# Performance work log

Hardware: AMD Instinct MI355X
Metric: run time of the kernel (lower is better)

The kernel has to match this reference:

```python
import jax, jax.numpy as jnp
import numpy as np

N, E = 50000, 400000          # nodes, edges
T, R = 4, 8                   # node types, relations (edge types)
H, DK = 8, 32                 # heads, head dim
DIN = DOUT = 256              # in/out feature dim (DOUT = H*DK)
SQRT_DK = float(np.sqrt(DK))


def setup_inputs() -> dict:
    key = jax.random.key(0)
    ks = jax.random.split(key, 12)
    f32 = jnp.float32
    return {
        "x": jax.random.normal(ks[0], (N, DIN), f32),
        "node_type": jax.random.randint(ks[1], (N,), 0, T, jnp.int32),
        "src": jax.random.randint(ks[2], (E,), 0, N, jnp.int32),
        "dst": jax.random.randint(ks[3], (E,), 0, N, jnp.int32),
        "etype": jax.random.randint(ks[4], (E,), 0, R, jnp.int32),
        "Wk": jax.random.normal(ks[5], (T, DOUT, DIN), f32) / np.sqrt(DIN).astype(np.float32),
        "bk": jnp.zeros((T, DOUT), f32),
        "Wq": jax.random.normal(ks[6], (T, DOUT, DIN), f32) / np.sqrt(DIN).astype(np.float32),
        "bq": jnp.zeros((T, DOUT), f32),
        "Wv": jax.random.normal(ks[7], (T, DOUT, DIN), f32) / np.sqrt(DIN).astype(np.float32),
        "bv": jnp.zeros((T, DOUT), f32),
        "Wa": jax.random.normal(ks[8], (T, DOUT, DOUT), f32) / np.sqrt(DOUT).astype(np.float32),
        "ba": jnp.zeros((T, DOUT), f32),
        "rel_pri": jnp.ones((R, H), f32),
        "rel_att": jax.random.normal(ks[9], (R, H, DK, DK), f32) / np.sqrt(DK).astype(np.float32),  # ~xavier
        "rel_msg": jax.random.normal(ks[10], (R, H, DK, DK), f32) / np.sqrt(DK).astype(np.float32),
        "skip": jnp.ones((T,), f32),
    }


def _typed_linear(h, W, b, ntype):
    # per-node-type linear: y_n = W[type_n] @ h_n + b[type_n]
    y = jnp.einsum('ni,tdi->ntd', h, W)                      # [N,T,D] (T is small)
    y = jnp.take_along_axis(y, ntype[:, None, None], axis=1)[:, 0]
    return y + b[ntype]


def _hgt_forward(x, node_type, src, dst, etype,
                 Wk, bk, Wq, bq, Wv, bv, Wa, ba,
                 rel_pri, rel_att, rel_msg, skip):
    # typed k/q/v projections -> [N,H,DK]
    K = _typed_linear(x, Wk, bk, node_type).reshape(N, H, DK)
    Q = _typed_linear(x, Wq, bq, node_type).reshape(N, H, DK)
    V = _typed_linear(x, Wv, bv, node_type).reshape(N, H, DK)

    k_e, q_e, v_e = K[src], Q[dst], V[src]                   # [E,H,DK] gathers

    # per-relation head transforms (loop over small fixed R, masked accumulate)
    key_e = jnp.zeros_like(k_e)
    msg_e = jnp.zeros_like(v_e)
    for r in range(R):
        m = (etype == r)[:, None, None].astype(x.dtype)
        key_e = key_e + m * jnp.einsum('ehd,hdf->ehf', k_e, rel_att[r])
        msg_e = msg_e + m * jnp.einsum('ehd,hdf->ehf', v_e, rel_msg[r])

    att = (q_e * key_e).sum(-1) * rel_pri[etype] / SQRT_DK   # [E,H]

    # softmax per (dst node, edge type) segment, then mean across edge types
    seg = dst * R + etype                                    # [E]
    S = N * R
    amax = jax.ops.segment_max(att, seg, num_segments=S)     # [S,H]
    ex = jnp.exp(att - amax[seg])
    denom = jax.ops.segment_sum(ex, seg, num_segments=S)
    w = ex / denom[seg]                                      # normalized attention [E,H]
    h_seg = jax.ops.segment_sum(w[:, :, None] * msg_e, seg, num_segments=S)  # [S,H,DK]
    cnt = jax.ops.segment_sum(jnp.ones((E,), x.dtype), seg, num_segments=S)  # [S]

    h_nr = h_seg.reshape(N, R, DOUT)
    present = (cnt.reshape(N, R) > 0).astype(x.dtype)        # which etypes hit each node
    t = h_nr.sum(1) / jnp.maximum(present.sum(1), 1.0)[:, None]  # cross_reducer='mean'

    trans = _typed_linear(t, Wa, ba, node_type)              # per-type output linear
    alpha = jax.nn.sigmoid(skip)[node_type][:, None]
    return trans * alpha + x * (1.0 - alpha)


def reference(x, node_type, src, dst, etype,
              Wk, bk, Wq, bq, Wv, bv, Wa, ba,
              rel_pri, rel_att, rel_msg, skip):
    return _hgt_forward(x, node_type, src, dst, etype,
                        Wk, bk, Wq, bq, Wv, bv, Wa, ba,
                        rel_pri, rel_att, rel_msg, skip)
```

## Files before the change

kernel.cpp:

```cpp
#include <hip/hip_runtime.h>
#include <math.h>
#include <stdint.h>

#define N_NODES 50000
#define N_EDGES 400000
#define N_T 4
#define N_R 8
#define N_H 8
#define DKD 32
#define D 256
#define TM 64
#define N_SEG (N_NODES * N_R)
#define PROJ_BLOCKS ((N_NODES + TM - 1) / TM + N_T)

typedef _Float16 h2 __attribute__((ext_vector_type(2)));
typedef _Float16 v8h __attribute__((ext_vector_type(8)));
typedef float v4f __attribute__((ext_vector_type(4)));
typedef unsigned short u16;

__device__ __forceinline__ u16 h2u(_Float16 h) { return __builtin_bit_cast(u16, h); }
__device__ __forceinline__ h2 u2h2(unsigned int u) { return __builtin_bit_cast(h2, u); }

#if __has_builtin(__builtin_amdgcn_fdot2)
__device__ __forceinline__ float fdot2f(h2 a, h2 b, float c) {
    return __builtin_amdgcn_fdot2(a, b, c, false);
}
#else
__device__ __forceinline__ float fdot2f(h2 a, h2 b, float c) {
    return c + (float)a[0] * (float)b[0] + (float)a[1] * (float)b[1];
}
#endif

__device__ __forceinline__ unsigned int pk16(float a, float b) {
#if __has_builtin(__builtin_amdgcn_cvt_pkrtz)
    return __builtin_bit_cast(unsigned int, __builtin_amdgcn_cvt_pkrtz(a, b));
#else
    return __builtin_bit_cast(unsigned int, h2{(_Float16)a, (_Float16)b});
#endif
}

struct Q4 { uint4 a, b, c, d; };

__device__ __forceinline__ float dot32q(const uint4* __restrict__ m, const Q4& q) {
    uint4 m0 = m[0], m1 = m[1], m2 = m[2], m3 = m[3];
    float s = 0.f;
    s = fdot2f(u2h2(m0.x), u2h2(q.a.x), s);
    s = fdot2f(u2h2(m0.y), u2h2(q.a.y), s);
    s = fdot2f(u2h2(m0.z), u2h2(q.a.z), s);
    s = fdot2f(u2h2(m0.w), u2h2(q.a.w), s);
    s = fdot2f(u2h2(m1.x), u2h2(q.b.x), s);
    s = fdot2f(u2h2(m1.y), u2h2(q.b.y), s);
    s = fdot2f(u2h2(m1.z), u2h2(q.b.z), s);
    s = fdot2f(u2h2(m1.w), u2h2(q.b.w), s);
    s = fdot2f(u2h2(m2.x), u2h2(q.c.x), s);
    s = fdot2f(u2h2(m2.y), u2h2(q.c.y), s);
    s = fdot2f(u2h2(m2.z), u2h2(q.c.z), s);
    s = fdot2f(u2h2(m2.w), u2h2(q.c.w), s);
    s = fdot2f(u2h2(m3.x), u2h2(q.d.x), s);
    s = fdot2f(u2h2(m3.y), u2h2(q.d.y), s);
    s = fdot2f(u2h2(m3.z), u2h2(q.d.z), s);
    s = fdot2f(u2h2(m3.w), u2h2(q.d.w), s);
    return s;
}

__global__ __launch_bounds__(256) void k_cvtW(
    const float4* __restrict__ w0, const float4* __restrict__ w1,
    const float4* __restrict__ w2, const float4* __restrict__ w3,
    ushort4* __restrict__ d, int n4each) {
    int i = blockIdx.x * 256 + threadIdx.x;
    if (i >= 4 * n4each) return;
    int sel = i / n4each, j = i - sel * n4each;
    const float4* s = (sel == 0) ? w0 : (sel == 1) ? w1 : (sel == 2) ? w2 : w3;
    float4 v = s[j];
    ushort4 o;
    o.x = h2u((_Float16)v.x); o.y = h2u((_Float16)v.y);
    o.z = h2u((_Float16)v.z); o.w = h2u((_Float16)v.w);
    d[i] = o;
}

__global__ __launch_bounds__(256) void k_cvt_att(const float4* __restrict__ s,
                                                 const float* __restrict__ pri,
                                                 ushort4* __restrict__ d, int n4) {
    int i = blockIdx.x * 256 + threadIdx.x;
    if (i >= n4) return;
    int mat = i >> 8;
    float sc = pri[mat] * 0.2550309305920868f;
    float4 v = s[i];
    ushort4 o;
    o.x = h2u((_Float16)(v.x * sc)); o.y = h2u((_Float16)(v.y * sc));
    o.z = h2u((_Float16)(v.z * sc)); o.w = h2u((_Float16)(v.w * sc));
    d[i] = o;
}

__global__ __launch_bounds__(256) void k_cvt_t(const float* __restrict__ s,
                                               u16* __restrict__ d) {
    int i = blockIdx.x * 256 + threadIdx.x;
    if (i >= N_R * N_H * DKD * DKD) return;
    int mat = i >> 10, w = i & 1023;
    int d0 = w >> 5, f = w & 31;
    d[(mat << 10) + f * DKD + d0] = h2u((_Float16)s[i]);
}

__global__ void k_hist(const int* __restrict__ nt, int* __restrict__ cnt) {
    int n = blockIdx.x * blockDim.x + threadIdx.x;
    if (n < N_NODES) atomicAdd(&cnt[nt[n]], 1);
}

__global__ void k_scan(const int* __restrict__ cnt, int* __restrict__ off,
                       int* __restrict__ toff) {
    int o = 0, to = 0;
    for (int t = 0; t < N_T; t++) {
        off[t] = o; toff[t] = to;
        o += cnt[t]; to += (cnt[t] + TM - 1) / TM;
    }
    off[N_T] = o; toff[N_T] = to;
}

__global__ void k_scatter(const int* __restrict__ nt, const int* __restrict__ off,
                          int* __restrict__ cur, int* __restrict__ order) {
    int n = blockIdx.x * blockDim.x + threadIdx.x;
    if (n >= N_NODES) return;
    int t = nt[n];
    int pos = off[t] + atomicAdd(&cur[t], 1);
    order[pos] = n;
}

__global__ void k_hist_seg(const int* __restrict__ dst, const int* __restrict__ et,
                           int* __restrict__ cnt) {
    int e = blockIdx.x * blockDim.x + threadIdx.x;
    if (e < N_EDGES) atomicAdd(&cnt[dst[e] * N_R + et[e]], 1);
}

__global__ __launch_bounds__(1024) void k_scan_l1(const int* __restrict__ cnt,
                                                  int* __restrict__ excl,
                                                  int* __restrict__ bsum) {
    __shared__ int sh[1024];
    int tid = threadIdx.x, i = blockIdx.x * 1024 + tid;
    int v = (i < N_SEG) ? cnt[i] : 0;
    sh[tid] = v;
    __syncthreads();
    #pragma unroll
    for (int ofs = 1; ofs < 1024; ofs <<= 1) {
        int t = (tid >= ofs) ? sh[tid - ofs] : 0;
        __syncthreads();
        sh[tid] += t;
        __syncthreads();
    }
    if (i < N_SEG) excl[i] = sh[tid] - v;
    if (tid == 1023) bsum[blockIdx.x] = sh[1023];
}

__global__ __launch_bounds__(512) void k_scan_l2(int* __restrict__ bsum, int NB) {
    __shared__ int sh[512];
    int tid = threadIdx.x;
    int v = (tid < NB) ? bsum[tid] : 0;
    sh[tid] = v;
    __syncthreads();
    #pragma unroll
    for (int ofs = 1; ofs < 512; ofs <<= 1) {
        int t = (tid >= ofs) ? sh[tid - ofs] : 0;
        __syncthreads();
        sh[tid] += t;
        __syncthreads();
    }
    if (tid < NB) bsum[tid] = sh[tid] - v;
}

__global__ void k_scan_l3(int* __restrict__ excl, const int* __restrict__ bsum) {
    int i = blockIdx.x * blockDim.x + threadIdx.x;
    if (i < N_SEG) excl[i] += bsum[i >> 10];
    else if (i == N_SEG) excl[N_SEG] = N_EDGES;
}

__global__ void k_scatter_seg(const int* __restrict__ src, const int* __restrict__ dst,
                              const int* __restrict__ et, const int* __restrict__ rp,
                              int* __restrict__ cur, int* __restrict__ esrc) {
    int e = blockIdx.x * blockDim.x + threadIdx.x;
    if (e >= N_EDGES) return;
    int sg = dst[e] * N_R + et[e];
    int pos = rp[sg] + atomicAdd(&cur[sg], 1);
    esrc[pos] = src[e];
}

__global__ __launch_bounds__(256) void k_proj(
    const float* __restrict__ x, const int* __restrict__ order,
    const int* __restrict__ off, const int* __restrict__ toff,
    const u16* __restrict__ Wkb, const float* __restrict__ bk,
    const u16* __restrict__ Wqb, const float* __restrict__ bq,
    const u16* __restrict__ Wvb, const float* __restrict__ bv,
    u16* __restrict__ Kb, u16* __restrict__ Qb, u16* __restrict__ Vb) {
    __shared__ __align__(16) u16 xs[TM][D + 8];
    int b = blockIdx.x;
    int t = -1;
    #pragma unroll
    for (int i = 0; i < N_T; i++)
        if (b >= toff[i] && b < toff[i + 1]) t = i;
    if (t < 0) return;
    int nodeBase = off[t] + (b - toff[t]) * TM;
    int count = min(TM, off[t + 1] - nodeBase);
    int tid = threadIdx.x;

    for (int j = tid; j < TM * (D / 4); j += 256) {
        int row = j >> 6, ch = j & 63;
        float4 v = {0.f, 0.f, 0.f, 0.f};
        if (row < count) {
            int g = order[nodeBase + row];
            v = *(const float4*)(x + (size_t)g * D + ch * 4);
        }
        ushort4 o;
        o.x = h2u((_Float16)v.x); o.y = h2u((_Float16)v.y);
        o.z = h2u((_Float16)v.z); o.w = h2u((_Float16)v.w);
        *(ushort4*)&xs[row][ch * 4] = o;
    }
    __syncthreads();

    int lane = tid & 63, wave = tid >> 6;
    int m = lane & 15, quad = lane >> 4;
    v8h a[8];
    #pragma unroll
    for (int ks = 0; ks < 8; ks++)
        a[ks] = *(const v8h*)&xs[wave * 16 + m][ks * 32 + quad * 8];

    int grow[4]; bool vrow[4];
    #pragma unroll
    for (int r = 0; r < 4; r++) {
        int rowi = wave * 16 + quad * 4 + r;
        vrow[r] = (rowi < count);
        grow[r] = vrow[r] ? order[nodeBase + rowi] : 0;
    }

    const u16* Ws[3] = {Wkb + (size_t)t * D * D, Wqb + (size_t)t * D * D, Wvb + (size_t)t * D * D};
    const float* Bs[3] = {bk + t * D, bq + t * D, bv + t * D};
    u16* Os[3] = {Kb, Qb, Vb};

    for (int p = 0; p < 3; p++) {
        const u16* W = Ws[p];
        for (int dt = 0; dt < 16; dt++) {
            int dcol = dt * 16 + m;
            v4f acc = {0.f, 0.f, 0.f, 0.f};
            #pragma unroll
            for (int ks = 0; ks < 8; ks++) {
                v8h bf = *(const v8h*)(W + (size_t)dcol * D + ks * 32 + quad * 8);
                acc = __builtin_amdgcn_mfma_f32_16x16x32_f16(a[ks], bf, acc, 0, 0, 0);
            }
            float bias = Bs[p][dcol];
            #pragma unroll
            for (int r = 0; r < 4; r++) {
                if (vrow[r])
                    Os[p][(size_t)grow[r] * D + dcol] = h2u((_Float16)(acc[r] + bias));
            }
        }
    }
}

__global__ __launch_bounds__(256) void k_fused(
    const u16* __restrict__ Kb, u16* QTb, const u16* __restrict__ Vb,
    const int* __restrict__ rowptr, const int* __restrict__ esrc,
    const u16* __restrict__ Ab, const u16* __restrict__ Mtb) {
    int tid = threadIdx.x;
    int n = blockIdx.x * 32 + (tid >> 3);
    if (n >= N_NODES) return;
    int h = tid & 7;
    int base = n * N_R;
    u16* qrow = QTb + (size_t)n * D + h * DKD;

    float macc[DKD];
    #pragma unroll
    for (int j = 0; j < DKD; j++) macc[j] = 0.f;
    float np = 0.f;

    int s0 = rowptr[base];
    for (int r = 0; r < N_R; r++) {
        int s1 = rowptr[base + r + 1];
        if (s0 < s1) {
            np += 1.f;
            Q4 q4;
            {
                const uint4* qp = (const uint4*)qrow;
                q4.a = qp[0]; q4.b = qp[1]; q4.c = qp[2]; q4.d = qp[3];
            }
            const uint4* Ar = (const uint4*)(Ab + ((size_t)(r * N_H + h) << 10));
            Q4 qt;
            {
                float t0, t1;
                t0 = dot32q(Ar + 0, q4);  t1 = dot32q(Ar + 4, q4);  qt.a.x = pk16(t0, t1);
                t0 = dot32q(Ar + 8, q4);  t1 = dot32q(Ar + 12, q4); qt.a.y = pk16(t0, t1);
                t0 = dot32q(Ar + 16, q4); t1 = dot32q(Ar + 20, q4); qt.a.z = pk16(t0, t1);
                t0 = dot32q(Ar + 24, q4); t1 = dot32q(Ar + 28, q4); qt.a.w = pk16(t0, t1);
                t0 = dot32q(Ar + 32, q4); t1 = dot32q(Ar + 36, q4); qt.b.x = pk16(t0, t1);
                t0 = dot32q(Ar + 40, q4); t1 = dot32q(Ar + 44, q4); qt.b.y = pk16(t0, t1);
                t0 = dot32q(Ar + 48, q4); t1 = dot32q(Ar + 52, q4); qt.b.z = pk16(t0, t1);
                t0 = dot32q(Ar + 56, q4); t1 = dot32q(Ar + 60, q4); qt.b.w = pk16(t0, t1);
                t0 = dot32q(Ar + 64, q4); t1 = dot32q(Ar + 68, q4); qt.c.x = pk16(t0, t1);
                t0 = dot32q(Ar + 72, q4); t1 = dot32q(Ar + 76, q4); qt.c.y = pk16(t0, t1);
                t0 = dot32q(Ar + 80, q4); t1 = dot32q(Ar + 84, q4); qt.c.z = pk16(t0, t1);
                t0 = dot32q(Ar + 88, q4); t1 = dot32q(Ar + 92, q4); qt.c.w = pk16(t0, t1);
                t0 = dot32q(Ar + 96, q4); t1 = dot32q(Ar + 100, q4); qt.d.x = pk16(t0, t1);
                t0 = dot32q(Ar + 104, q4); t1 = dot32q(Ar + 108, q4); qt.d.y = pk16(t0, t1);
                t0 = dot32q(Ar + 112, q4); t1 = dot32q(Ar + 116, q4); qt.d.z = pk16(t0, t1);
                t0 = dot32q(Ar + 120, q4); t1 = dot32q(Ar + 124, q4); qt.d.w = pk16(t0, t1);
            }
            float den = 0.f;
            float U[DKD];
            #pragma unroll
            for (int j = 0; j < DKD; j++) U[j] = 0.f;
            for (int e = s0; e < s1; e++) {
                int s = esrc[e];
                const uint4* kp = (const uint4*)(Kb + (size_t)s * D + h * DKD);
                const uint4* vp = (const uint4*)(Vb + (size_t)s * D + h * DKD);
                Q4 kv; kv.a = kp[0]; kv.b = kp[1]; kv.c = kp[2]; kv.d = kp[3];
                uint4 v0 = vp[0], v1 = vp[1], v2 = vp[2], v3 = vp[3];
                float p = 0.f;
                p = fdot2f(u2h2(kv.a.x), u2h2(qt.a.x), p);
                p = fdot2f(u2h2(kv.a.y), u2h2(qt.a.y), p);
                p = fdot2f(u2h2(kv.a.z), u2h2(qt.a.z), p);
                p = fdot2f(u2h2(kv.a.w), u2h2(qt.a.w), p);
                p = fdot2f(u2h2(kv.b.x), u2h2(qt.b.x), p);
                p = fdot2f(u2h2(kv.b.y), u2h2(qt.b.y), p);
                p = fdot2f(u2h2(kv.b.z), u2h2(qt.b.z), p);
                p = fdot2f(u2h2(kv.b.w), u2h2(qt.b.w), p);
                p = fdot2f(u2h2(kv.c.x), u2h2(qt.c.x), p);
                p = fdot2f(u2h2(kv.c.y), u2h2(qt.c.y), p);
                p = fdot2f(u2h2(kv.c.z), u2h2(qt.c.z), p);
                p = fdot2f(u2h2(kv.c.w), u2h2(qt.c.w), p);
                p = fdot2f(u2h2(kv.d.x), u2h2(qt.d.x), p);
                p = fdot2f(u2h2(kv.d.y), u2h2(qt.d.y), p);
                p = fdot2f(u2h2(kv.d.z), u2h2(qt.d.z), p);
                p = fdot2f(u2h2(kv.d.w), u2h2(qt.d.w), p);
                float ex = exp2f(p);
                den += ex;
#define UACC(VV, J0) { h2 _t = u2h2(VV); U[J0] += ex * (float)_t[0]; U[J0 + 1] += ex * (float)_t[1]; }
                UACC(v0.x, 0)  UACC(v0.y, 2)  UACC(v0.z, 4)  UACC(v0.w, 6)
                UACC(v1.x, 8)  UACC(v1.y, 10) UACC(v1.z, 12) UACC(v1.w, 14)
                UACC(v2.x, 16) UACC(v2.y, 18) UACC(v2.z, 20) UACC(v2.w, 22)
                UACC(v3.x, 24) UACC(v3.y, 26) UACC(v3.z, 28) UACC(v3.w, 30)
#undef UACC
            }
            float invd = 1.f / den;
            Q4 uh;
            uh.a.x = pk16(U[0] * invd, U[1] * invd);
            uh.a.y = pk16(U[2] * invd, U[3] * invd);
            uh.a.z = pk16(U[4] * invd, U[5] * invd);
            uh.a.w = pk16(U[6] * invd, U[7] * invd);
            uh.b.x = pk16(U[8] * invd, U[9] * invd);
            uh.b.y = pk16(U[10] * invd, U[11] * invd);
            uh.b.z = pk16(U[12] * invd, U[13] * invd);
            uh.b.w = pk16(U[14] * invd, U[15] * invd);
            uh.c.x = pk16(U[16] * invd, U[17] * invd);
            uh.c.y = pk16(U[18] * invd, U[19] * invd);
            uh.c.z = pk16(U[20] * invd, U[21] * invd);
            uh.c.w = pk16(U[22] * invd, U[23] * invd);
            uh.d.x = pk16(U[24] * invd, U[25] * invd);
            uh.d.y = pk16(U[26] * invd, U[27] * invd);
            uh.d.z = pk16(U[28] * invd, U[29] * invd);
            uh.d.w = pk16(U[30] * invd, U[31] * invd);
            const uint4* Mr = (const uint4*)(Mtb + ((size_t)(r * N_H + h) << 10));
            #pragma unroll
            for (int f = 0; f < DKD; f++)
                macc[f] += dot32q(Mr + f * 4, uh);
        }
        s0 = s1;
    }

    float invp = (np > 0.f) ? 1.f / np : 1.f;
    uint4 o0, o1, o2, o3;
    o0.x = pk16(macc[0] * invp, macc[1] * invp);
    o0.y = pk16(macc[2] * invp, macc[3] * invp);
    o0.z = pk16(macc[4] * invp, macc[5] * invp);
    o0.w = pk16(macc[6] * invp, macc[7] * invp);
    o1.x = pk16(macc[8] * invp, macc[9] * invp);
    o1.y = pk16(macc[10] * invp, macc[11] * invp);
    o1.z = pk16(macc[12] * invp, macc[13] * invp);
    o1.w = pk16(macc[14] * invp, macc[15] * invp);
    o2.x = pk16(macc[16] * invp, macc[17] * invp);
    o2.y = pk16(macc[18] * invp, macc[19] * invp);
    o2.z = pk16(macc[20] * invp, macc[21] * invp);
    o2.w = pk16(macc[22] * invp, macc[23] * invp);
    o3.x = pk16(macc[24] * invp, macc[25] * invp);
    o3.y = pk16(macc[26] * invp, macc[27] * invp);
    o3.z = pk16(macc[28] * invp, macc[29] * invp);
    o3.w = pk16(macc[30] * invp, macc[31] * invp);
    uint4* op = (uint4*)qrow;
    op[0] = o0; op[1] = o1; op[2] = o2; op[3] = o3;
}

__global__ __launch_bounds__(256) void k_out(
    const u16* __restrict__ TBF, const float* __restrict__ x,
    const int* __restrict__ order, const int* __restrict__ off, const int* __restrict__ toff,
    const u16* __restrict__ Wab, const float* __restrict__ ba,
    const float* __restrict__ skip, float* __restrict__ out) {
    __shared__ __align__(16) u16 xs[TM][D + 8];
    int b = blockIdx.x;
    int t = -1;
    #pragma unroll
    for (int i = 0; i < N_T; i++)
        if (b >= toff[i] && b < toff[i + 1]) t = i;
    if (t < 0) return;
    int nodeBase = off[t] + (b - toff[t]) * TM;
    int count = min(TM, off[t + 1] - nodeBase);
    int tid = threadIdx.x;

    for (int j = tid; j < TM * 32; j += 256) {
        int row = j >> 5, ch = j & 31;
        ushort4 z = {0, 0, 0, 0};
        if (row < count) {
            int g = order[nodeBase + row];
            const ushort4* p = (const ushort4*)(TBF + (size_t)g * D + ch * 8);
            *(ushort4*)&xs[row][ch * 8] = p[0];
            *(ushort4*)&xs[row][ch * 8 + 4] = p[1];
        } else {
            *(ushort4*)&xs[row][ch * 8] = z;
            *(ushort4*)&xs[row][ch * 8 + 4] = z;
        }
    }
    __syncthreads();

    int lane = tid & 63, wave = tid >> 6;
    int m = lane & 15, quad = lane >> 4;
    v8h a[8];
    #pragma unroll
    for (int ks = 0; ks < 8; ks++)
        a[ks] = *(const v8h*)&xs[wave * 16 + m][ks * 32 + quad * 8];

    int grow[4]; bool vrow[4];
    #pragma unroll
    for (int r = 0; r < 4; r++) {
        int rowi = wave * 16 + quad * 4 + r;
        vrow[r] = (rowi < count);
        grow[r] = vrow[r] ? order[nodeBase + rowi] : 0;
    }

    float sv = skip[t];
    float alpha = 1.f / (1.f + __expf(-sv));
    float beta = 1.f - alpha;
    const u16* W = Wab + (size_t)t * D * D;

    for (int dt = 0; dt < 16; dt++) {
        int dcol = dt * 16 + m;
        v4f acc = {0.f, 0.f, 0.f, 0.f};
        #pragma unroll
        for (int ks = 0; ks < 8; ks++) {
            v8h bf = *(const v8h*)(W + (size_t)dcol * D + ks * 32 + quad * 8);
            acc = __builtin_amdgcn_mfma_f32_16x16x32_f16(a[ks], bf, acc, 0, 0, 0);
        }
        float bias = ba[t * D + dcol];
        #pragma unroll
        for (int r = 0; r < 4; r++) {
            if (vrow[r]) {
                size_t o = (size_t)grow[r] * D + dcol;
                out[o] = alpha * (acc[r] + bias) + beta * x[o];
            }
        }
    }
}

extern "C" void kernel_launch(void* const* d_in, const int* in_sizes, int n_in,
                              void* d_out, int out_size, void* d_ws, size_t ws_size,
                              hipStream_t stream) {
    const float* x       = (const float*)d_in[0];
    const int* node_type = (const int*)d_in[1];
    const int* src       = (const int*)d_in[2];
    const int* dst       = (const int*)d_in[3];
    const int* etype     = (const int*)d_in[4];
    const float* Wk = (const float*)d_in[5];
    const float* bk = (const float*)d_in[6];
    const float* Wq = (const float*)d_in[7];
    const float* bq = (const float*)d_in[8];
    const float* Wv = (const float*)d_in[9];
    const float* bv = (const float*)d_in[10];
    const float* Wa = (const float*)d_in[11];
    const float* ba = (const float*)d_in[12];
    const float* rel_pri = (const float*)d_in[13];
    const float* rel_att = (const float*)d_in[14];
    const float* rel_msg = (const float*)d_in[15];
    const float* skip    = (const float*)d_in[16];
    float* out = (float*)d_out;
    char* ws = (char*)d_ws;

    const size_t SZH = (size_t)N_NODES * D * 2;
    const size_t WSZ = (size_t)N_T * D * D;
    const size_t RSZ = (size_t)N_R * N_H * DKD * DKD;
    u16* Kb  = (u16*)(ws);
    u16* Qb  = (u16*)(ws + SZH);
    u16* Vb  = (u16*)(ws + 2 * SZH);
    u16* TBF = Qb;
    u16* Wkb = (u16*)(ws + 3 * SZH);
    u16* Wqb = Wkb + WSZ;
    u16* Wvb = Wqb + WSZ;
    u16* Wab = Wvb + WSZ;
    u16* Ab  = Wab + WSZ;
    u16* Mtb = Ab + RSZ;
    int* order = (int*)(Mtb + RSZ);
    int* small = order + N_NODES;
    int* cnt  = small;
    int* cur  = small + 4;
    int* offp = small + 8;
    int* toffp= small + 13;

    char* ob = (char*)d_out;
    int* rowptr_seg = (int*)ob;
    int* cnt_seg    = rowptr_seg + (N_SEG + 16);
    int* cur_seg    = cnt_seg + N_SEG;
    int* esrc       = cur_seg + N_SEG;
    int* bsum       = esrc + N_EDGES;

    hipMemsetAsync(small, 0, 8 * sizeof(int), stream);
    hipMemsetAsync(cnt_seg, 0, 2 * (size_t)N_SEG * sizeof(int), stream);

    k_cvtW<<<(4 * (WSZ / 4) + 255) / 256, 256, 0, stream>>>(
        (const float4*)Wk, (const float4*)Wq, (const float4*)Wv, (const float4*)Wa,
        (ushort4*)Wkb, WSZ / 4);
    k_cvt_att<<<(RSZ / 4 + 255) / 256, 256, 0, stream>>>(
        (const float4*)rel_att, rel_pri, (ushort4*)Ab, RSZ / 4);
    k_cvt_t<<<(RSZ + 255) / 256, 256, 0, stream>>>(rel_msg, Mtb);

    k_hist<<<(N_NODES + 255) / 256, 256, 0, stream>>>(node_type, cnt);
    k_scan<<<1, 1, 0, stream>>>(cnt, offp, toffp);
    k_scatter<<<(N_NODES + 255) / 256, 256, 0, stream>>>(node_type, offp, cur, order);

    const int NB = (N_SEG + 1023) / 1024;
    k_hist_seg<<<(N_EDGES + 255) / 256, 256, 0, stream>>>(dst, etype, cnt_seg);
    k_scan_l1<<<NB, 1024, 0, stream>>>(cnt_seg, rowptr_seg, bsum);
    k_scan_l2<<<1, 512, 0, stream>>>(bsum, NB);
    k_scan_l3<<<(N_SEG + 1 + 255) / 256, 256, 0, stream>>>(rowptr_seg, bsum);
    k_scatter_seg<<<(N_EDGES + 255) / 256, 256, 0, stream>>>(src, dst, etype,
                                                             rowptr_seg, cur_seg, esrc);

    k_proj<<<PROJ_BLOCKS, 256, 0, stream>>>(x, order, offp, toffp,
                                            Wkb, bk, Wqb, bq, Wvb, bv, Kb, Qb, Vb);

    k_fused<<<(N_NODES + 31) / 32, 256, 0, stream>>>(Kb, Qb, Vb, rowptr_seg, esrc,
                                                     Ab, Mtb);

    k_out<<<PROJ_BLOCKS, 256, 0, stream>>>(TBF, x, order, offp, toffp,
                                           Wab, ba, skip, out);
}
```

Measured before the change: 2.248 ms.

## Assign one wavefront per node and split edges and relation matmuls across lanes

```diff
diff --git a/kernel.cpp b/kernel.cpp
--- a/kernel.cpp
+++ b/kernel.cpp
@@ -257,131 +257,127 @@
     const u16* __restrict__ Kb, u16* QTb, const u16* __restrict__ Vb,
     const int* __restrict__ rowptr, const int* __restrict__ esrc,
     const u16* __restrict__ Ab, const u16* __restrict__ Mtb) {
-    int tid = threadIdx.x;
-    int n = blockIdx.x * 32 + (tid >> 3);
+    int wave = threadIdx.x >> 6, lane = threadIdx.x & 63;
+    int n = blockIdx.x * 4 + wave;
     if (n >= N_NODES) return;
-    int h = tid & 7;
+    int j = lane >> 3, h = lane & 7;
     int base = n * N_R;
-    u16* qrow = QTb + (size_t)n * D + h * DKD;
-
-    float macc[DKD];
-    #pragma unroll
-    for (int j = 0; j < DKD; j++) macc[j] = 0.f;
+
+    int bnd[N_R + 1];
+    #pragma unroll
+    for (int i = 0; i <= N_R; i++)
+        bnd[i] = __builtin_amdgcn_readfirstlane(rowptr[base + i]);
+
+    Q4 q4;
+    {
+        const uint4* qp = (const uint4*)(QTb + (size_t)n * D + h * DKD);
+        q4.a = qp[0]; q4.b = qp[1]; q4.c = qp[2]; q4.d = qp[3];
+    }
+
+    float macc[4] = {0.f, 0.f, 0.f, 0.f};
     float np = 0.f;
 
-    int s0 = rowptr[base];
     for (int r = 0; r < N_R; r++) {
-        int s1 = rowptr[base + r + 1];
-        if (s0 < s1) {
-            np += 1.f;
-            Q4 q4;
-            {
-                const uint4* qp = (const uint4*)qrow;
-                q4.a = qp[0]; q4.b = qp[1]; q4.c = qp[2]; q4.d = qp[3];
-            }
-            const uint4* Ar = (const uint4*)(Ab + ((size_t)(r * N_H + h) << 10));
-            Q4 qt;
-            {
-                float t0, t1;
-                t0 = dot32q(Ar + 0, q4);  t1 = dot32q(Ar + 4, q4);  qt.a.x = pk16(t0, t1);
-                t0 = dot32q(Ar + 8, q4);  t1 = dot32q(Ar + 12, q4); qt.a.y = pk16(t0, t1);
-                t0 = dot32q(Ar + 16, q4); t1 = dot32q(Ar + 20, q4); qt.a.z = pk16(t0, t1);
-                t0 = dot32q(Ar + 24, q4); t1 = dot32q(Ar + 28, q4); qt.a.w = pk16(t0, t1);
-                t0 = dot32q(Ar + 32, q4); t1 = dot32q(Ar + 36, q4); qt.b.x = pk16(t0, t1);
-                t0 = dot32q(Ar + 40, q4); t1 = dot32q(Ar + 44, q4); qt.b.y = pk16(t0, t1);
-                t0 = dot32q(Ar + 48, q4); t1 = dot32q(Ar + 52, q4); qt.b.z = pk16(t0, t1);
-                t0 = dot32q(Ar + 56, q4); t1 = dot32q(Ar + 60, q4); qt.b.w = pk16(t0, t1);
-                t0 = dot32q(Ar + 64, q4); t1 = dot32q(Ar + 68, q4); qt.c.x = pk16(t0, t1);
-                t0 = dot32q(Ar + 72, q4); t1 = dot32q(Ar + 76, q4); qt.c.y = pk16(t0, t1);
-                t0 = dot32q(Ar + 80, q4); t1 = dot32q(Ar + 84, q4); qt.c.z = pk16(t0, t1);
-                t0 = dot32q(Ar + 88, q4); t1 = dot32q(Ar + 92, q4); qt.c.w = pk16(t0, t1);
-                t0 = dot32q(Ar + 96, q4); t1 = dot32q(Ar + 100, q4); qt.d.x = pk16(t0, t1);
-                t0 = dot32q(Ar + 104, q4); t1 = dot32q(Ar + 108, q4); qt.d.y = pk16(t0, t1);
-                t0 = dot32q(Ar + 112, q4); t1 = dot32q(Ar + 116, q4); qt.d.z = pk16(t0, t1);
-                t0 = dot32q(Ar + 120, q4); t1 = dot32q(Ar + 124, q4); qt.d.w = pk16(t0, t1);
-            }
-            float den = 0.f;
-            float U[DKD];
-            #pragma unroll
-            for (int j = 0; j < DKD; j++) U[j] = 0.f;
-            for (int e = s0; e < s1; e++) {
-                int s = esrc[e];
-                const uint4* kp = (const uint4*)(Kb + (size_t)s * D + h * DKD);
-                const uint4* vp = (const uint4*)(Vb + (size_t)s * D + h * DKD);
-                Q4 kv; kv.a = kp[0]; kv.b = kp[1]; kv.c = kp[2]; kv.d = kp[3];
-                uint4 v0 = vp[0], v1 = vp[1], v2 = vp[2], v3 = vp[3];
-                float p = 0.f;
-                p = fdot2f(u2h2(kv.a.x), u2h2(qt.a.x), p);
-                p = fdot2f(u2h2(kv.a.y), u2h2(qt.a.y), p);
-                p = fdot2f(u2h2(kv.a.z), u2h2(qt.a.z), p);
-                p = fdot2f(u2h2(kv.a.w), u2h2(qt.a.w), p);
-                p = fdot2f(u2h2(kv.b.x), u2h2(qt.b.x), p);
-                p = fdot2f(u2h2(kv.b.y), u2h2(qt.b.y), p);
-                p = fdot2f(u2h2(kv.b.z), u2h2(qt.b.z), p);
-                p = fdot2f(u2h2(kv.b.w), u2h2(qt.b.w), p);
-                p = fdot2f(u2h2(kv.c.x), u2h2(qt.c.x), p);
-                p = fdot2f(u2h2(kv.c.y), u2h2(qt.c.y), p);
-                p = fdot2f(u2h2(kv.c.z), u2h2(qt.c.z), p);
-                p = fdot2f(u2h2(kv.c.w), u2h2(qt.c.w), p);
-                p = fdot2f(u2h2(kv.d.x), u2h2(qt.d.x), p);
-                p = fdot2f(u2h2(kv.d.y), u2h2(qt.d.y), p);
-                p = fdot2f(u2h2(kv.d.z), u2h2(qt.d.z), p);
-                p = fdot2f(u2h2(kv.d.w), u2h2(qt.d.w), p);
-                float ex = exp2f(p);
-                den += ex;
+        int s0 = bnd[r], s1 = bnd[r + 1];
+
+        const uint4* Ar = (const uint4*)(Ab + ((size_t)(r * N_H + h) << 10));
+        float t0 = dot32q(Ar + (4 * j + 0) * 4, q4);
+        float t1 = dot32q(Ar + (4 * j + 1) * 4, q4);
+        float t2 = dot32q(Ar + (4 * j + 2) * 4, q4);
+        float t3 = dot32q(Ar + (4 * j + 3) * 4, q4);
+        unsigned int qp0 = pk16(t0, t1), qp1 = pk16(t2, t3);
+        Q4 qt;
+        qt.a.x = __shfl(qp0, 0 * 8 + h); qt.a.y = __shfl(qp1, 0 * 8 + h);
+        qt.a.z = __shfl(qp0, 1 * 8 + h); qt.a.w = __shfl(qp1, 1 * 8 + h);
+        qt.b.x = __shfl(qp0, 2 * 8 + h); qt.b.y = __shfl(qp1, 2 * 8 + h);
+        qt.b.z = __shfl(qp0, 3 * 8 + h); qt.b.w = __shfl(qp1, 3 * 8 + h);
+        qt.c.x = __shfl(qp0, 4 * 8 + h); qt.c.y = __shfl(qp1, 4 * 8 + h);
+        qt.c.z = __shfl(qp0, 5 * 8 + h); qt.c.w = __shfl(qp1, 5 * 8 + h);
+        qt.d.x = __shfl(qp0, 6 * 8 + h); qt.d.y = __shfl(qp1, 6 * 8 + h);
+        qt.d.z = __shfl(qp0, 7 * 8 + h); qt.d.w = __shfl(qp1, 7 * 8 + h);
+
+        if (s0 >= s1) continue;
+        np += 1.f;
+
+        float den_p = 0.f;
+        float U[DKD];
+        #pragma unroll
+        for (int i = 0; i < DKD; i++) U[i] = 0.f;
+        for (int b0 = s0; b0 < s1; b0 += 8) {
+            int e = b0 + j;
+            bool act = (e < s1);
+            int s = esrc[act ? e : s0];
+            const uint4* kp = (const uint4*)(Kb + (size_t)s * D + h * DKD);
+            const uint4* vp = (const uint4*)(Vb + (size_t)s * D + h * DKD);
+            Q4 kv; kv.a = kp[0]; kv.b = kp[1]; kv.c = kp[2]; kv.d = kp[3];
+            uint4 v0 = vp[0], v1 = vp[1], v2 = vp[2], v3 = vp[3];
+            float p = 0.f;
+            p = fdot2f(u2h2(kv.a.x), u2h2(qt.a.x), p);
+            p = fdot2f(u2h2(kv.a.y), u2h2(qt.a.y), p);
+            p = fdot2f(u2h2(kv.a.z), u2h2(qt.a.z), p);
+            p = fdot2f(u2h2(kv.a.w), u2h2(qt.a.w), p);
+            p = fdot2f(u2h2(kv.b.x), u2h2(qt.b.x), p);
+            p = fdot2f(u2h2(kv.b.y), u2h2(qt.b.y), p);
+            p = fdot2f(u2h2(kv.b.z), u2h2(qt.b.z), p);
+            p = fdot2f(u2h2(kv.b.w), u2h2(qt.b.w), p);
+            p = fdot2f(u2h2(kv.c.x), u2h2(qt.c.x), p);
+            p = fdot2f(u2h2(kv.c.y), u2h2(qt.c.y), p);
+            p = fdot2f(u2h2(kv.c.z), u2h2(qt.c.z), p);
+            p = fdot2f(u2h2(kv.c.w), u2h2(qt.c.w), p);
+            p = fdot2f(u2h2(kv.d.x), u2h2(qt.d.x), p);
+            p = fdot2f(u2h2(kv.d.y), u2h2(qt.d.y), p);
+            p = fdot2f(u2h2(kv.d.z), u2h2(qt.d.z), p);
+            p = fdot2f(u2h2(kv.d.w), u2h2(qt.d.w), p);
+            float ex = act ? exp2f(p) : 0.f;
+            den_p += ex;
 #define UACC(VV, J0) { h2 _t = u2h2(VV); U[J0] += ex * (float)_t[0]; U[J0 + 1] += ex * (float)_t[1]; }
-                UACC(v0.x, 0)  UACC(v0.y, 2)  UACC(v0.z, 4)  UACC(v0.w, 6)
-                UACC(v1.x, 8)  UACC(v1.y, 10) UACC(v1.z, 12) UACC(v1.w, 14)
-                UACC(v2.x, 16) UACC(v2.y, 18) UACC(v2.z, 20) UACC(v2.w, 22)
-                UACC(v3.x, 24) UACC(v3.y, 26) UACC(v3.z, 28) UACC(v3.w, 30)
+            UACC(v0.x, 0)  UACC(v0.y, 2)  UACC(v0.z, 4)  UACC(v0.w, 6)
+            UACC(v1.x, 8)  UACC(v1.y, 10) UACC(v1.z, 12) UACC(v1.w, 14)
+            UACC(v2.x, 16) UACC(v2.y, 18) UACC(v2.z, 20) UACC(v2.w, 22)
+            UACC(v3.x, 24) UACC(v3.y, 26) UACC(v3.z, 28) UACC(v3.w, 30)
 #undef UACC
-            }
-            float invd = 1.f / den;
-            Q4 uh;
-            uh.a.x = pk16(U[0] * invd, U[1] * invd);
-            uh.a.y = pk16(U[2] * invd, U[3] * invd);
-            uh.a.z = pk16(U[4] * invd, U[5] * invd);
-            uh.a.w = pk16(U[6] * invd, U[7] * invd);
-            uh.b.x = pk16(U[8] * invd, U[9] * invd);
-            uh.b.y = pk16(U[10] * invd, U[11] * invd);
-            uh.b.z = pk16(U[12] * invd, U[13] * invd);
-            uh.b.w = pk16(U[14] * invd, U[15] * invd);
-            uh.c.x = pk16(U[16] * invd, U[17] * invd);
-            uh.c.y = pk16(U[18] * invd, U[19] * invd);
-            uh.c.z = pk16(U[20] * invd, U[21] * invd);
-            uh.c.w = pk16(U[22] * invd, U[23] * invd);
-            uh.d.x = pk16(U[24] * invd, U[25] * invd);
-            uh.d.y = pk16(U[26] * invd, U[27] * invd);
-            uh.d.z = pk16(U[28] * invd, U[29] * invd);
-            uh.d.w = pk16(U[30] * invd, U[31] * invd);
-            const uint4* Mr = (const uint4*)(Mtb + ((size_t)(r * N_H + h) << 10));
-            #pragma unroll
-            for (int f = 0; f < DKD; f++)
-                macc[f] += dot32q(Mr + f * 4, uh);
-        }
-        s0 = s1;
+        }
+
+        den_p += __shfl_xor(den_p, 8);
+        den_p += __shfl_xor(den_p, 16);
+        den_p += __shfl_xor(den_p, 32);
+        #pragma unroll
+        for (int i = 0; i < DKD; i++) {
+            U[i] += __shfl_xor(U[i], 8);
+            U[i] += __shfl_xor(U[i], 16);
+            U[i] += __shfl_xor(U[i], 32);
+        }
+        float invd = 1.f / den_p;
+        Q4 uh;
+        uh.a.x = pk16(U[0] * invd, U[1] * invd);
+        uh.a.y = pk16(U[2] * invd, U[3] * invd);
+        uh.a.z = pk16(U[4] * invd, U[5] * invd);
+        uh.a.w = pk16(U[6] * invd, U[7] * invd);
+        uh.b.x = pk16(U[8] * invd, U[9] * invd);
+        uh.b.y = pk16(U[10] * invd, U[11] * invd);
+        uh.b.z = pk16(U[12] * invd, U[13] * invd);
+        uh.b.w = pk16(U[14] * invd, U[15] * invd);
+        uh.c.x = pk16(U[16] * invd, U[17] * invd);
+        uh.c.y = pk16(U[18] * invd, U[19] * invd);
+        uh.c.z = pk16(U[20] * invd, U[21] * invd);
+        uh.c.w = pk16(U[22] * invd, U[23] * invd);
+        uh.d.x = pk16(U[24] * invd, U[25] * invd);
+        uh.d.y = pk16(U[26] * invd, U[27] * invd);
+        uh.d.z = pk16(U[28] * invd, U[29] * invd);
+        uh.d.w = pk16(U[30] * invd, U[31] * invd);
+
+        const uint4* Mr = (const uint4*)(Mtb + ((size_t)(r * N_H + h) << 10));
+        macc[0] += dot32q(Mr + (4 * j + 0) * 4, uh);
+        macc[1] += dot32q(Mr + (4 * j + 1) * 4, uh);
+        macc[2] += dot32q(Mr + (4 * j + 2) * 4, uh);
+        macc[3] += dot32q(Mr + (4 * j + 3) * 4, uh);
     }
 
     float invp = (np > 0.f) ? 1.f / np : 1.f;
-    uint4 o0, o1, o2, o3;
-    o0.x = pk16(macc[0] * invp, macc[1] * invp);
-    o0.y = pk16(macc[2] * invp, macc[3] * invp);
-    o0.z = pk16(macc[4] * invp, macc[5] * invp);
-    o0.w = pk16(macc[6] * invp, macc[7] * invp);
-    o1.x = pk16(macc[8] * invp, macc[9] * invp);
-    o1.y = pk16(macc[10] * invp, macc[11] * invp);
-    o1.z = pk16(macc[12] * invp, macc[13] * invp);
-    o1.w = pk16(macc[14] * invp, macc[15] * invp);
-    o2.x = pk16(macc[16] * invp, macc[17] * invp);
-    o2.y = pk16(macc[18] * invp, macc[19] * invp);
-    o2.z = pk16(macc[20] * invp, macc[21] * invp);
-    o2.w = pk16(macc[22] * invp, macc[23] * invp);
-    o3.x = pk16(macc[24] * invp, macc[25] * invp);
-    o3.y = pk16(macc[26] * invp, macc[27] * invp);
-    o3.z = pk16(macc[28] * invp, macc[29] * invp);
-    o3.w = pk16(macc[30] * invp, macc[31] * invp);
-    uint4* op = (uint4*)qrow;
-    op[0] = o0; op[1] = o1; op[2] = o2; op[3] = o3;
+    unsigned int w0 = pk16(macc[0] * invp, macc[1] * invp);
+    unsigned int w1 = pk16(macc[2] * invp, macc[3] * invp);
+    uint2 ow = {w0, w1};
+    *(uint2*)(QTb + (size_t)n * D + h * DKD + 4 * j) = ow;
 }
 
 __global__ __launch_bounds__(256) void k_out(
@@ -529,8 +525,8 @@
     k_proj<<<PROJ_BLOCKS, 256, 0, stream>>>(x, order, offp, toffp,
                                             Wkb, bk, Wqb, bq, Wvb, bv, Kb, Qb, Vb);
 
-    k_fused<<<(N_NODES + 31) / 32, 256, 0, stream>>>(Kb, Qb, Vb, rowptr_seg, esrc,
-                                                     Ab, Mtb);
+    k_fused<<<(N_NODES + 3) / 4, 256, 0, stream>>>(Kb, Qb, Vb, rowptr_seg, esrc,
+                                                   Ab, Mtb);
 
     k_out<<<PROJ_BLOCKS, 256, 0, stream>>>(TBF, x, order, offp, toffp,
                                            Wab, ba, skip, out);
```

Result: slower. 2.351 ms (+4.6%).
